# Kernel tuning notes

Hardware: AMD Instinct MI355X
Metric: run time of the kernel (lower is better)

## Reference

```python
import jax, jax.numpy as jnp
import numpy as np

B, S, D, O, R, E = 4, 2048, 4096, 4096, 16, 8
SCALING = 32.0 / 16.0  # lora_alpha / lora_rank


def setup_inputs() -> dict:
    key = jax.random.key(0)
    ks = jax.random.split(key, 7)
    x = jax.random.normal(ks[0], (B, S, D), dtype=jnp.float32)
    W_base = jax.random.normal(ks[1], (O, D), dtype=jnp.float32) * 0.02
    b_base = jnp.zeros((O,), dtype=jnp.float32)
    A_w = jax.random.normal(ks[2], (R, D), dtype=jnp.float32) * 0.02     # lora_A weight
    B_w = jax.random.normal(ks[3], (O, R), dtype=jnp.float32) * 0.02     # lora_B weight
    router_w = jax.random.normal(ks[4], (E, D), dtype=jnp.float32) * 0.02  # router weight (core_router=False -> acts on x)
    cores = jax.random.normal(ks[5], (E, R, R), dtype=jnp.float32)       # expert rank x rank cores
    return {"x": x, "W_base": W_base, "b_base": b_base, "A_w": A_w,
            "B_w": B_w, "router_w": router_w, "cores": cores}


def reference(x, W_base, b_base, A_w, B_w, router_w, cores):
    # base linear: [B,S,O]
    result = jnp.einsum('bsd,od->bso', x, W_base) + b_base
    # lora down-projection (dropout=0 -> identity): [B,S,R]
    ax = jnp.einsum('bsd,rd->bsr', x, A_w)
    # router on x (core_router=False): softmax over experts -> [B,S,E]
    probs = jax.nn.softmax(jnp.einsum('bsd,ed->bse', x, router_w), axis=-1)
    # per-token weighted core applied to ax WITHOUT materializing [B,S,R,R]:
    # first ax through each expert core [B,S,E,R], then weight-reduce over experts.
    per_expert = jnp.einsum('bsr,erq->bseq', ax, cores)
    mixed = jnp.einsum('bseq,bse->bsq', per_expert, probs)  # [B,S,R]
    result = result + jnp.einsum('bsr,or->bso', mixed, B_w) * SCALING
    return result
```

## Files before the change

kernel.cpp:

```cpp
#include <hip/hip_runtime.h>
#include <stdint.h>

#define D_DIM 4096
#define O_DIM 4096
#define M_DIM 8192
#define SCALE_F 2.0f
#define BK 32
#define NKT 128

typedef __attribute__((ext_vector_type(4))) float f32x4;
typedef __attribute__((ext_vector_type(8))) __bf16 bf16x8;
typedef __attribute__((ext_vector_type(8))) unsigned short u16x8;

__device__ __forceinline__ unsigned short f32_to_bf16_bits(float f) {
    union { float f; uint32_t u; } v; v.f = f;
    return (unsigned short)((v.u + 0x7FFFu + ((v.u >> 16) & 1u)) >> 16);
}

__device__ __forceinline__ float dot4(f32x4 a, f32x4 b) {
    return fmaf(a.x, b.x, fmaf(a.y, b.y, fmaf(a.z, b.z, a.w * b.w)));
}

__device__ __forceinline__ int swz(int b) { return b ^ (((b >> 7) & 7) << 4); }

__global__ __launch_bounds__(256) void convert_bf16_kernel(const float* __restrict__ src,
                                                           unsigned short* __restrict__ dst,
                                                           int n4) {
    int stride = gridDim.x * blockDim.x;
    for (int i = blockIdx.x * blockDim.x + threadIdx.x; i < n4; i += stride) {
        f32x4 v = ((const f32x4*)src)[i];
        ushort4 o;
        o.x = f32_to_bf16_bits(v.x);
        o.y = f32_to_bf16_bits(v.y);
        o.z = f32_to_bf16_bits(v.z);
        o.w = f32_to_bf16_bits(v.w);
        ((ushort4*)dst)[i] = o;
    }
}

__global__ __launch_bounds__(256) void partial_mixed_kernel(const float* __restrict__ x,
                                                            const float* __restrict__ A_w,
                                                            const float* __restrict__ router_w,
                                                            unsigned short* __restrict__ xbf,
                                                            float* __restrict__ ypart) {
    __shared__ __align__(16) float Xc[32][132];
    __shared__ __align__(16) float Wc[24][132];

    const int tid = threadIdx.x;
    const int t0 = blockIdx.x * 32;
    const int d0 = blockIdx.y * 512;

    const int tg = tid >> 3;
    const int og = tid & 7;
    float acc0 = 0.f, acc1 = 0.f, acc2 = 0.f;

    for (int sub = 0; sub < 4; ++sub) {
        const int dbase = d0 + sub * 128;
        __syncthreads();
        #pragma unroll
        for (int i = 0; i < 4; ++i) {
            int idx = i * 256 + tid;
            int t = idx >> 5, dq = idx & 31;
            f32x4 v = *(const f32x4*)&x[(size_t)(t0 + t) * D_DIM + dbase + dq * 4];
            *(f32x4*)&Xc[t][dq * 4] = v;
            ushort4 o;
            o.x = f32_to_bf16_bits(v.x);
            o.y = f32_to_bf16_bits(v.y);
            o.z = f32_to_bf16_bits(v.z);
            o.w = f32_to_bf16_bits(v.w);
            *(ushort4*)&xbf[(size_t)(t0 + t) * D_DIM + dbase + dq * 4] = o;
        }
        #pragma unroll
        for (int i = 0; i < 3; ++i) {
            int idx = i * 256 + tid;
            int r = idx >> 5, dq = idx & 31;
            const float* src = (r < 16) ? (A_w + (size_t)r * D_DIM)
                                        : (router_w + (size_t)(r - 16) * D_DIM);
            *(f32x4*)&Wc[r][dq * 4] = *(const f32x4*)&src[dbase + dq * 4];
        }
        __syncthreads();
        #pragma unroll
        for (int dq = 0; dq < 32; ++dq) {
            f32x4 xv = *(const f32x4*)&Xc[tg][dq * 4];
            acc0 += dot4(xv, *(const f32x4*)&Wc[og * 3 + 0][dq * 4]);
            acc1 += dot4(xv, *(const f32x4*)&Wc[og * 3 + 1][dq * 4]);
            acc2 += dot4(xv, *(const f32x4*)&Wc[og * 3 + 2][dq * 4]);
        }
    }
    float* dst = ypart + (((size_t)blockIdx.y * 256 + blockIdx.x) * 32 + tg) * 24 + og * 3;
    dst[0] = acc0; dst[1] = acc1; dst[2] = acc2;
}

__global__ __launch_bounds__(128) void finalize_mixed_kernel(const float* __restrict__ ypart,
                                                             const float* __restrict__ cores,
                                                             float* __restrict__ mixbuf) {
    __shared__ __align__(16) float Cs[2048];
    const int tid = threadIdx.x;
    #pragma unroll
    for (int i = 0; i < 4; ++i) {
        int idx = i * 128 + tid;
        ((f32x4*)Cs)[idx] = ((const f32x4*)cores)[idx];
    }
    __syncthreads();

    const int tok = blockIdx.x * 128 + tid;
    const int tile = tok >> 5, t = tok & 31;

    float y[24];
    #pragma unroll
    for (int j = 0; j < 24; ++j) y[j] = 0.f;
    for (int ds = 0; ds < 8; ++ds) {
        const float* src = ypart + (((size_t)ds * 256 + tile) * 32 + t) * 24;
        #pragma unroll
        for (int j = 0; j < 24; ++j) y[j] += src[j];
    }

    float mx = y[16];
    #pragma unroll
    for (int e = 1; e < 8; ++e) mx = fmaxf(mx, y[16 + e]);
    float p[8], psum = 0.f;
    #pragma unroll
    for (int e = 0; e < 8; ++e) { p[e] = __expf(y[16 + e] - mx); psum += p[e]; }
    const float inv = 1.0f / psum;

    float outq[16];
    #pragma unroll
    for (int q = 0; q < 16; ++q) outq[q] = 0.f;
    for (int e = 0; e < 8; ++e) {
        const float pe = p[e] * inv;
        #pragma unroll
        for (int r = 0; r < 16; ++r) {
            const float ar = y[r] * pe;
            #pragma unroll
            for (int q = 0; q < 16; ++q)
                outq[q] = fmaf(ar, Cs[(e * 16 + r) * 16 + q], outq[q]);
        }
    }
    #pragma unroll
    for (int q = 0; q < 4; ++q) {
        f32x4 v = {outq[q * 4 + 0], outq[q * 4 + 1], outq[q * 4 + 2], outq[q * 4 + 3]};
        *(f32x4*)&mixbuf[(size_t)tok * 16 + q * 4] = v;
    }
}

__global__ __launch_bounds__(512, 2) void gemm_kernel(const unsigned short* __restrict__ xbf,
                                                      const unsigned short* __restrict__ wbf,
                                                      const float* __restrict__ bias,
                                                      const float* __restrict__ Bw,
                                                      const float* __restrict__ mixbuf,
                                                      float* __restrict__ out) {
    __shared__ __align__(16) unsigned short lds[4][2][256 * 32];

    const int bid = blockIdx.x;
    const int xcd = bid & 7;
    const int lid = bid >> 3;
    const int tm = (lid >> 4) * 8 + xcd;
    const int tn = lid & 15;
    const int m0 = tm * 256, n0 = tn * 256;

    const int tid = threadIdx.x;
    const int wave = tid >> 6, lane = tid & 63;
    const int wr = wave >> 2, wcn = wave & 3;

    int aoff[2], boff[2];
    #pragma unroll
    for (int u = 0; u < 2; ++u) {
        int c = u * 512 + tid;
        int g = swz(c * 16);
        int grow = g >> 6, gc8 = (g >> 4) & 3;
        aoff[u] = (m0 + grow) * D_DIM + gc8 * 8;
        boff[u] = (n0 + grow) * D_DIM + gc8 * 8;
    }

    const int tA = lane & 15, kq = lane >> 4;
    int aRd[8], bRd[4];
    #pragma unroll
    for (int mi = 0; mi < 8; ++mi)
        aRd[mi] = swz((wr * 128 + mi * 16 + tA) * 64 + kq * 16);
    #pragma unroll
    for (int ni = 0; ni < 4; ++ni)
        bRd[ni] = swz((wcn * 64 + ni * 16 + tA) * 64 + kq * 16);

    f32x4 acc[8][4];
    const f32x4 fz = {0.f, 0.f, 0.f, 0.f};
    #pragma unroll
    for (int mi = 0; mi < 8; ++mi)
        #pragma unroll
        for (int ni = 0; ni < 4; ++ni) acc[mi][ni] = fz;

#define STAGE_UNIT(sb, kt, u, isA)                                                        \
    do {                                                                                  \
        const unsigned short* gsrc =                                                      \
            (isA) ? (xbf + aoff[u] + (kt)*BK) : (wbf + boff[u] + (kt)*BK);                \
        __builtin_amdgcn_global_load_lds(                                                 \
            (const __attribute__((address_space(1))) void*)gsrc,                          \
            (__attribute__((address_space(3))) void*)(&lds[sb][(isA) ? 0 : 1]             \
                                                         [((u)*512 + wave * 64) * 8]),    \
            16, 0, 0);                                                                    \
    } while (0)

    #pragma unroll
    for (int kt = 0; kt < 3; ++kt) {
        STAGE_UNIT(kt, kt, 0, 1);
        STAGE_UNIT(kt, kt, 1, 1);
        STAGE_UNIT(kt, kt, 0, 0);
        STAGE_UNIT(kt, kt, 1, 0);
    }
    asm volatile("s_waitcnt vmcnt(8)" ::: "memory");
    __builtin_amdgcn_s_barrier();
    asm volatile("" ::: "memory");

    for (int jj = 0; jj < 32; ++jj) {
        #pragma unroll
        for (int i = 0; i < 4; ++i) {
            const int j = jj * 4 + i;
            const int buf = i;
            const int kt = j + 3;
            const int sbuf = (i + 3) & 3;
            const char* Ab = (const char*)&lds[buf][0][0];
            const char* Bb = (const char*)&lds[buf][1][0];

            bf16x8 b0 = __builtin_bit_cast(bf16x8, *(const u16x8*)(Bb + bRd[0]));
            bf16x8 b1 = __builtin_bit_cast(bf16x8, *(const u16x8*)(Bb + bRd[1]));
            bf16x8 b2 = __builtin_bit_cast(bf16x8, *(const u16x8*)(Bb + bRd[2]));
            bf16x8 b3 = __builtin_bit_cast(bf16x8, *(const u16x8*)(Bb + bRd[3]));
            bf16x8 a0 = __builtin_bit_cast(bf16x8, *(const u16x8*)(Ab + aRd[0]));
            bf16x8 a1 = __builtin_bit_cast(bf16x8, *(const u16x8*)(Ab + aRd[1]));
            bf16x8 a2 = __builtin_bit_cast(bf16x8, *(const u16x8*)(Ab + aRd[2]));
            bf16x8 a3 = __builtin_bit_cast(bf16x8, *(const u16x8*)(Ab + aRd[3]));
            if (kt < NKT) {
                STAGE_UNIT(sbuf, kt, 0, 1);
                STAGE_UNIT(sbuf, kt, 1, 1);
                STAGE_UNIT(sbuf, kt, 0, 0);
                STAGE_UNIT(sbuf, kt, 1, 0);
            }
            asm volatile("" ::: "memory");
            __builtin_amdgcn_s_barrier();
            asm volatile("s_waitcnt lgkmcnt(0)" ::: "memory");
            __builtin_amdgcn_s_setprio(1);
            acc[0][0] = __builtin_amdgcn_mfma_f32_16x16x32_bf16(a0, b0, acc[0][0], 0, 0, 0);
            acc[0][1] = __builtin_amdgcn_mfma_f32_16x16x32_bf16(a0, b1, acc[0][1], 0, 0, 0);
            acc[0][2] = __builtin_amdgcn_mfma_f32_16x16x32_bf16(a0, b2, acc[0][2], 0, 0, 0);
            acc[0][3] = __builtin_amdgcn_mfma_f32_16x16x32_bf16(a0, b3, acc[0][3], 0, 0, 0);
            acc[1][0] = __builtin_amdgcn_mfma_f32_16x16x32_bf16(a1, b0, acc[1][0], 0, 0, 0);
            acc[1][1] = __builtin_amdgcn_mfma_f32_16x16x32_bf16(a1, b1, acc[1][1], 0, 0, 0);
            acc[1][2] = __builtin_amdgcn_mfma_f32_16x16x32_bf16(a1, b2, acc[1][2], 0, 0, 0);
            acc[1][3] = __builtin_amdgcn_mfma_f32_16x16x32_bf16(a1, b3, acc[1][3], 0, 0, 0);
            acc[2][0] = __builtin_amdgcn_mfma_f32_16x16x32_bf16(a2, b0, acc[2][0], 0, 0, 0);
            acc[2][1] = __builtin_amdgcn_mfma_f32_16x16x32_bf16(a2, b1, acc[2][1], 0, 0, 0);
            acc[2][2] = __builtin_amdgcn_mfma_f32_16x16x32_bf16(a2, b2, acc[2][2], 0, 0, 0);
            acc[2][3] = __builtin_amdgcn_mfma_f32_16x16x32_bf16(a2, b3, acc[2][3], 0, 0, 0);
            acc[3][0] = __builtin_amdgcn_mfma_f32_16x16x32_bf16(a3, b0, acc[3][0], 0, 0, 0);
            acc[3][1] = __builtin_amdgcn_mfma_f32_16x16x32_bf16(a3, b1, acc[3][1], 0, 0, 0);
            acc[3][2] = __builtin_amdgcn_mfma_f32_16x16x32_bf16(a3, b2, acc[3][2], 0, 0, 0);
            acc[3][3] = __builtin_amdgcn_mfma_f32_16x16x32_bf16(a3, b3, acc[3][3], 0, 0, 0);
            __builtin_amdgcn_s_setprio(0);

            bf16x8 a4 = __builtin_bit_cast(bf16x8, *(const u16x8*)(Ab + aRd[4]));
            bf16x8 a5 = __builtin_bit_cast(bf16x8, *(const u16x8*)(Ab + aRd[5]));
            bf16x8 a6 = __builtin_bit_cast(bf16x8, *(const u16x8*)(Ab + aRd[6]));
            bf16x8 a7 = __builtin_bit_cast(bf16x8, *(const u16x8*)(Ab + aRd[7]));
            asm volatile("s_waitcnt lgkmcnt(0)" ::: "memory");
            __builtin_amdgcn_s_setprio(1);
            acc[4][0] = __builtin_amdgcn_mfma_f32_16x16x32_bf16(a4, b0, acc[4][0], 0, 0, 0);
            acc[4][1] = __builtin_amdgcn_mfma_f32_16x16x32_bf16(a4, b1, acc[4][1], 0, 0, 0);
            acc[4][2] = __builtin_amdgcn_mfma_f32_16x16x32_bf16(a4, b2, acc[4][2], 0, 0, 0);
            acc[4][3] = __builtin_amdgcn_mfma_f32_16x16x32_bf16(a4, b3, acc[4][3], 0, 0, 0);
            acc[5][0] = __builtin_amdgcn_mfma_f32_16x16x32_bf16(a5, b0, acc[5][0], 0, 0, 0);
            acc[5][1] = __builtin_amdgcn_mfma_f32_16x16x32_bf16(a5, b1, acc[5][1], 0, 0, 0);
            acc[5][2] = __builtin_amdgcn_mfma_f32_16x16x32_bf16(a5, b2, acc[5][2], 0, 0, 0);
            acc[5][3] = __builtin_amdgcn_mfma_f32_16x16x32_bf16(a5, b3, acc[5][3], 0, 0, 0);
            acc[6][0] = __builtin_amdgcn_mfma_f32_16x16x32_bf16(a6, b0, acc[6][0], 0, 0, 0);
            acc[6][1] = __builtin_amdgcn_mfma_f32_16x16x32_bf16(a6, b1, acc[6][1], 0, 0, 0);
            acc[6][2] = __builtin_amdgcn_mfma_f32_16x16x32_bf16(a6, b2, acc[6][2], 0, 0, 0);
            acc[6][3] = __builtin_amdgcn_mfma_f32_16x16x32_bf16(a6, b3, acc[6][3], 0, 0, 0);
            acc[7][0] = __builtin_amdgcn_mfma_f32_16x16x32_bf16(a7, b0, acc[7][0], 0, 0, 0);
            acc[7][1] = __builtin_amdgcn_mfma_f32_16x16x32_bf16(a7, b1, acc[7][1], 0, 0, 0);
            acc[7][2] = __builtin_amdgcn_mfma_f32_16x16x32_bf16(a7, b2, acc[7][2], 0, 0, 0);
            acc[7][3] = __builtin_amdgcn_mfma_f32_16x16x32_bf16(a7, b3, acc[7][3], 0, 0, 0);
            __builtin_amdgcn_s_setprio(0);
            asm volatile("s_waitcnt vmcnt(8)" ::: "memory");
            __builtin_amdgcn_s_barrier();
            asm volatile("" ::: "memory");
        }
    }
#undef STAGE_UNIT

    const int colq = lane & 15, rq = lane >> 4;
    f32x4 bwv[4][4];
    float bcol[4];
    #pragma unroll
    for (int ni = 0; ni < 4; ++ni) {
        const int col = n0 + wcn * 64 + ni * 16 + colq;
        bcol[ni] = bias[col];
        #pragma unroll
        for (int k = 0; k < 4; ++k) bwv[ni][k] = *(const f32x4*)&Bw[(size_t)col * 16 + k * 4];
    }
    #pragma unroll
    for (int mi = 0; mi < 8; ++mi) {
        #pragma unroll
        for (int j = 0; j < 4; ++j) {
            const int row = m0 + wr * 128 + mi * 16 + rq * 4 + j;
            const f32x4* mx = (const f32x4*)&mixbuf[(size_t)row * 16];
            const f32x4 m0v = mx[0], m1v = mx[1], m2v = mx[2], m3v = mx[3];
            #pragma unroll
            for (int ni = 0; ni < 4; ++ni) {
                const int col = n0 + wcn * 64 + ni * 16 + colq;
                const float lora = dot4(m0v, bwv[ni][0]) + dot4(m1v, bwv[ni][1]) +
                                   dot4(m2v, bwv[ni][2]) + dot4(m3v, bwv[ni][3]);
                out[(size_t)row * O_DIM + col] = acc[mi][ni][j] + bcol[ni] + SCALE_F * lora;
            }
        }
    }
}

extern "C" void kernel_launch(void* const* d_in, const int* in_sizes, int n_in,
                              void* d_out, int out_size, void* d_ws, size_t ws_size,
                              hipStream_t stream) {
    const float* x        = (const float*)d_in[0];
    const float* W_base   = (const float*)d_in[1];
    const float* b_base   = (const float*)d_in[2];
    const float* A_w      = (const float*)d_in[3];
    const float* B_w      = (const float*)d_in[4];
    const float* router_w = (const float*)d_in[5];
    const float* cores    = (const float*)d_in[6];
    float* out = (float*)d_out;

    char* ws = (char*)d_ws;
    unsigned short* xbf = (unsigned short*)ws;
    unsigned short* wbf = (unsigned short*)(ws + (size_t)M_DIM * D_DIM * 2);
    char* after_w = ws + (size_t)M_DIM * D_DIM * 2 + (size_t)O_DIM * D_DIM * 2;
    float* mixbuf = (float*)after_w;
    float* ypart  = (float*)(after_w + (size_t)M_DIM * 16 * 4);

    convert_bf16_kernel<<<2048, 256, 0, stream>>>(W_base, wbf, (O_DIM * D_DIM) / 4);
    partial_mixed_kernel<<<dim3(256, 8), 256, 0, stream>>>(x, A_w, router_w, xbf, ypart);
    finalize_mixed_kernel<<<64, 128, 0, stream>>>(ypart, cores, mixbuf);
    gemm_kernel<<<512, 512, 0, stream>>>(xbf, wbf, b_base, B_w, mixbuf, out);
}
```

Measured before the change: 345.5 us.

## Merge W conversion with partial mixing kernel and split GEMM k-loop staging

Folds the W_base bf16 conversion and the x down-projection/router partials into one launch, with blocks split by index, so the two independent prologue jobs run concurrently and one launch is saved. The GEMM main loop is reorganised: B and A tile prefetches are issued in two halves around an extra barrier. The final four k-steps are peeled out with shrinking vmcnt waits instead of a per-iteration kt<NKT branch. The extra barrier per k-step may cost more than the finer interleaving gains.

```diff
diff --git a/kernel.cpp b/kernel.cpp
--- a/kernel.cpp
+++ b/kernel.cpp
@@ -23,32 +23,36 @@
 
 __device__ __forceinline__ int swz(int b) { return b ^ (((b >> 7) & 7) << 4); }
 
-__global__ __launch_bounds__(256) void convert_bf16_kernel(const float* __restrict__ src,
-                                                           unsigned short* __restrict__ dst,
-                                                           int n4) {
-    int stride = gridDim.x * blockDim.x;
-    for (int i = blockIdx.x * blockDim.x + threadIdx.x; i < n4; i += stride) {
-        f32x4 v = ((const f32x4*)src)[i];
-        ushort4 o;
-        o.x = f32_to_bf16_bits(v.x);
-        o.y = f32_to_bf16_bits(v.y);
-        o.z = f32_to_bf16_bits(v.z);
-        o.w = f32_to_bf16_bits(v.w);
-        ((ushort4*)dst)[i] = o;
-    }
-}
-
-__global__ __launch_bounds__(256) void partial_mixed_kernel(const float* __restrict__ x,
-                                                            const float* __restrict__ A_w,
-                                                            const float* __restrict__ router_w,
-                                                            unsigned short* __restrict__ xbf,
-                                                            float* __restrict__ ypart) {
+__global__ __launch_bounds__(256) void pre_kernel(const float* __restrict__ x,
+                                                  const float* __restrict__ W_base,
+                                                  const float* __restrict__ A_w,
+                                                  const float* __restrict__ router_w,
+                                                  unsigned short* __restrict__ xbf,
+                                                  unsigned short* __restrict__ wbf,
+                                                  float* __restrict__ ypart) {
     __shared__ __align__(16) float Xc[32][132];
     __shared__ __align__(16) float Wc[24][132];
 
     const int tid = threadIdx.x;
-    const int t0 = blockIdx.x * 32;
-    const int d0 = blockIdx.y * 512;
+
+    if (blockIdx.x < 2048) {
+        const int n4 = (O_DIM * D_DIM) / 4;
+        const int stride = 2048 * 256;
+        for (int i = blockIdx.x * 256 + tid; i < n4; i += stride) {
+            f32x4 v = ((const f32x4*)W_base)[i];
+            ushort4 o;
+            o.x = f32_to_bf16_bits(v.x);
+            o.y = f32_to_bf16_bits(v.y);
+            o.z = f32_to_bf16_bits(v.z);
+            o.w = f32_to_bf16_bits(v.w);
+            ((ushort4*)wbf)[i] = o;
+        }
+        return;
+    }
+
+    const int b = blockIdx.x - 2048;
+    const int t0 = (b & 255) * 32;
+    const int d0 = (b >> 8) * 512;
 
     const int tg = tid >> 3;
     const int og = tid & 7;
@@ -87,7 +91,7 @@
             acc2 += dot4(xv, *(const f32x4*)&Wc[og * 3 + 2][dq * 4]);
         }
     }
-    float* dst = ypart + (((size_t)blockIdx.y * 256 + blockIdx.x) * 32 + tg) * 24 + og * 3;
+    float* dst = ypart + (((size_t)(b >> 8) * 256 + (b & 255)) * 32 + tg) * 24 + og * 3;
     dst[0] = acc0; dst[1] = acc1; dst[2] = acc2;
 }
 
@@ -199,6 +203,80 @@
             16, 0, 0);                                                                    \
     } while (0)
 
+#define K_ITER(BUF, SBUF, KT, STG, VMC)                                                   \
+    {                                                                                     \
+        const char* Ab = (const char*)&lds[BUF][0][0];                                    \
+        const char* Bb = (const char*)&lds[BUF][1][0];                                    \
+        bf16x8 b0 = __builtin_bit_cast(bf16x8, *(const u16x8*)(Bb + bRd[0]));             \
+        bf16x8 b1 = __builtin_bit_cast(bf16x8, *(const u16x8*)(Bb + bRd[1]));             \
+        bf16x8 b2 = __builtin_bit_cast(bf16x8, *(const u16x8*)(Bb + bRd[2]));             \
+        bf16x8 b3 = __builtin_bit_cast(bf16x8, *(const u16x8*)(Bb + bRd[3]));             \
+        bf16x8 a0 = __builtin_bit_cast(bf16x8, *(const u16x8*)(Ab + aRd[0]));             \
+        bf16x8 a1 = __builtin_bit_cast(bf16x8, *(const u16x8*)(Ab + aRd[1]));             \
+        bf16x8 a2 = __builtin_bit_cast(bf16x8, *(const u16x8*)(Ab + aRd[2]));             \
+        bf16x8 a3 = __builtin_bit_cast(bf16x8, *(const u16x8*)(Ab + aRd[3]));             \
+        if (STG) {                                                                        \
+            STAGE_UNIT(SBUF, KT, 0, 1);                                                   \
+            STAGE_UNIT(SBUF, KT, 1, 1);                                                   \
+        }                                                                                 \
+        asm volatile("" ::: "memory");                                                    \
+        __builtin_amdgcn_s_barrier();                                                     \
+        asm volatile("s_waitcnt lgkmcnt(0)" ::: "memory");                                \
+        __builtin_amdgcn_s_setprio(1);                                                    \
+        acc[0][0] = __builtin_amdgcn_mfma_f32_16x16x32_bf16(a0, b0, acc[0][0], 0, 0, 0);  \
+        acc[0][1] = __builtin_amdgcn_mfma_f32_16x16x32_bf16(a0, b1, acc[0][1], 0, 0, 0);  \
+        acc[0][2] = __builtin_amdgcn_mfma_f32_16x16x32_bf16(a0, b2, acc[0][2], 0, 0, 0);  \
+        acc[0][3] = __builtin_amdgcn_mfma_f32_16x16x32_bf16(a0, b3, acc[0][3], 0, 0, 0);  \
+        acc[1][0] = __builtin_amdgcn_mfma_f32_16x16x32_bf16(a1, b0, acc[1][0], 0, 0, 0);  \
+        acc[1][1] = __builtin_amdgcn_mfma_f32_16x16x32_bf16(a1, b1, acc[1][1], 0, 0, 0);  \
+        acc[1][2] = __builtin_amdgcn_mfma_f32_16x16x32_bf16(a1, b2, acc[1][2], 0, 0, 0);  \
+        acc[1][3] = __builtin_amdgcn_mfma_f32_16x16x32_bf16(a1, b3, acc[1][3], 0, 0, 0);  \
+        acc[2][0] = __builtin_amdgcn_mfma_f32_16x16x32_bf16(a2, b0, acc[2][0], 0, 0, 0);  \
+        acc[2][1] = __builtin_amdgcn_mfma_f32_16x16x32_bf16(a2, b1, acc[2][1], 0, 0, 0);  \
+        acc[2][2] = __builtin_amdgcn_mfma_f32_16x16x32_bf16(a2, b2, acc[2][2], 0, 0, 0);  \
+        acc[2][3] = __builtin_amdgcn_mfma_f32_16x16x32_bf16(a2, b3, acc[2][3], 0, 0, 0);  \
+        acc[3][0] = __builtin_amdgcn_mfma_f32_16x16x32_bf16(a3, b0, acc[3][0], 0, 0, 0);  \
+        acc[3][1] = __builtin_amdgcn_mfma_f32_16x16x32_bf16(a3, b1, acc[3][1], 0, 0, 0);  \
+        acc[3][2] = __builtin_amdgcn_mfma_f32_16x16x32_bf16(a3, b2, acc[3][2], 0, 0, 0);  \
+        acc[3][3] = __builtin_amdgcn_mfma_f32_16x16x32_bf16(a3, b3, acc[3][3], 0, 0, 0);  \
+        __builtin_amdgcn_s_setprio(0);                                                    \
+        asm volatile("" ::: "memory");                                                    \
+        __builtin_amdgcn_s_barrier();                                                     \
+        asm volatile("" ::: "memory");                                                    \
+        bf16x8 a4 = __builtin_bit_cast(bf16x8, *(const u16x8*)(Ab + aRd[4]));             \
+        bf16x8 a5 = __builtin_bit_cast(bf16x8, *(const u16x8*)(Ab + aRd[5]));             \
+        bf16x8 a6 = __builtin_bit_cast(bf16x8, *(const u16x8*)(Ab + aRd[6]));             \
+        bf16x8 a7 = __builtin_bit_cast(bf16x8, *(const u16x8*)(Ab + aRd[7]));             \
+        if (STG) {                                                                        \
+            STAGE_UNIT(SBUF, KT, 0, 0);                                                   \
+            STAGE_UNIT(SBUF, KT, 1, 0);                                                   \
+        }                                                                                 \
+        asm volatile("s_waitcnt vmcnt(" #VMC ")" ::: "memory");                           \
+        __builtin_amdgcn_s_barrier();                                                     \
+        asm volatile("s_waitcnt lgkmcnt(0)" ::: "memory");                                \
+        __builtin_amdgcn_s_setprio(1);                                                    \
+        acc[4][0] = __builtin_amdgcn_mfma_f32_16x16x32_bf16(a4, b0, acc[4][0], 0, 0, 0);  \
+        acc[4][1] = __builtin_amdgcn_mfma_f32_16x16x32_bf16(a4, b1, acc[4][1], 0, 0, 0);  \
+        acc[4][2] = __builtin_amdgcn_mfma_f32_16x16x32_bf16(a4, b2, acc[4][2], 0, 0, 0);  \
+        acc[4][3] = __builtin_amdgcn_mfma_f32_16x16x32_bf16(a4, b3, acc[4][3], 0, 0, 0);  \
+        acc[5][0] = __builtin_amdgcn_mfma_f32_16x16x32_bf16(a5, b0, acc[5][0], 0, 0, 0);  \
+        acc[5][1] = __builtin_amdgcn_mfma_f32_16x16x32_bf16(a5, b1, acc[5][1], 0, 0, 0);  \
+        acc[5][2] = __builtin_amdgcn_mfma_f32_16x16x32_bf16(a5, b2, acc[5][2], 0, 0, 0);  \
+        acc[5][3] = __builtin_amdgcn_mfma_f32_16x16x32_bf16(a5, b3, acc[5][3], 0, 0, 0);  \
+        acc[6][0] = __builtin_amdgcn_mfma_f32_16x16x32_bf16(a6, b0, acc[6][0], 0, 0, 0);  \
+        acc[6][1] = __builtin_amdgcn_mfma_f32_16x16x32_bf16(a6, b1, acc[6][1], 0, 0, 0);  \
+        acc[6][2] = __builtin_amdgcn_mfma_f32_16x16x32_bf16(a6, b2, acc[6][2], 0, 0, 0);  \
+        acc[6][3] = __builtin_amdgcn_mfma_f32_16x16x32_bf16(a6, b3, acc[6][3], 0, 0, 0);  \
+        acc[7][0] = __builtin_amdgcn_mfma_f32_16x16x32_bf16(a7, b0, acc[7][0], 0, 0, 0);  \
+        acc[7][1] = __builtin_amdgcn_mfma_f32_16x16x32_bf16(a7, b1, acc[7][1], 0, 0, 0);  \
+        acc[7][2] = __builtin_amdgcn_mfma_f32_16x16x32_bf16(a7, b2, acc[7][2], 0, 0, 0);  \
+        acc[7][3] = __builtin_amdgcn_mfma_f32_16x16x32_bf16(a7, b3, acc[7][3], 0, 0, 0);  \
+        __builtin_amdgcn_s_setprio(0);                                                    \
+        asm volatile("" ::: "memory");                                                    \
+        __builtin_amdgcn_s_barrier();                                                     \
+        asm volatile("" ::: "memory");                                                    \
+    }
+
     #pragma unroll
     for (int kt = 0; kt < 3; ++kt) {
         STAGE_UNIT(kt, kt, 0, 1);
@@ -210,80 +288,19 @@
     __builtin_amdgcn_s_barrier();
     asm volatile("" ::: "memory");
 
-    for (int jj = 0; jj < 32; ++jj) {
+    for (int jj = 0; jj < 31; ++jj) {
         #pragma unroll
         for (int i = 0; i < 4; ++i) {
             const int j = jj * 4 + i;
-            const int buf = i;
             const int kt = j + 3;
-            const int sbuf = (i + 3) & 3;
-            const char* Ab = (const char*)&lds[buf][0][0];
-            const char* Bb = (const char*)&lds[buf][1][0];
-
-            bf16x8 b0 = __builtin_bit_cast(bf16x8, *(const u16x8*)(Bb + bRd[0]));
-            bf16x8 b1 = __builtin_bit_cast(bf16x8, *(const u16x8*)(Bb + bRd[1]));
-            bf16x8 b2 = __builtin_bit_cast(bf16x8, *(const u16x8*)(Bb + bRd[2]));
-            bf16x8 b3 = __builtin_bit_cast(bf16x8, *(const u16x8*)(Bb + bRd[3]));
-            bf16x8 a0 = __builtin_bit_cast(bf16x8, *(const u16x8*)(Ab + aRd[0]));
-            bf16x8 a1 = __builtin_bit_cast(bf16x8, *(const u16x8*)(Ab + aRd[1]));
-            bf16x8 a2 = __builtin_bit_cast(bf16x8, *(const u16x8*)(Ab + aRd[2]));
-            bf16x8 a3 = __builtin_bit_cast(bf16x8, *(const u16x8*)(Ab + aRd[3]));
-            if (kt < NKT) {
-                STAGE_UNIT(sbuf, kt, 0, 1);
-                STAGE_UNIT(sbuf, kt, 1, 1);
-                STAGE_UNIT(sbuf, kt, 0, 0);
-                STAGE_UNIT(sbuf, kt, 1, 0);
-            }
-            asm volatile("" ::: "memory");
-            __builtin_amdgcn_s_barrier();
-            asm volatile("s_waitcnt lgkmcnt(0)" ::: "memory");
-            __builtin_amdgcn_s_setprio(1);
-            acc[0][0] = __builtin_amdgcn_mfma_f32_16x16x32_bf16(a0, b0, acc[0][0], 0, 0, 0);
-            acc[0][1] = __builtin_amdgcn_mfma_f32_16x16x32_bf16(a0, b1, acc[0][1], 0, 0, 0);
-            acc[0][2] = __builtin_amdgcn_mfma_f32_16x16x32_bf16(a0, b2, acc[0][2], 0, 0, 0);
-            acc[0][3] = __builtin_amdgcn_mfma_f32_16x16x32_bf16(a0, b3, acc[0][3], 0, 0, 0);
-            acc[1][0] = __builtin_amdgcn_mfma_f32_16x16x32_bf16(a1, b0, acc[1][0], 0, 0, 0);
-            acc[1][1] = __builtin_amdgcn_mfma_f32_16x16x32_bf16(a1, b1, acc[1][1], 0, 0, 0);
-            acc[1][2] = __builtin_amdgcn_mfma_f32_16x16x32_bf16(a1, b2, acc[1][2], 0, 0, 0);
-            acc[1][3] = __builtin_amdgcn_mfma_f32_16x16x32_bf16(a1, b3, acc[1][3], 0, 0, 0);
-            acc[2][0] = __builtin_amdgcn_mfma_f32_16x16x32_bf16(a2, b0, acc[2][0], 0, 0, 0);
-            acc[2][1] = __builtin_amdgcn_mfma_f32_16x16x32_bf16(a2, b1, acc[2][1], 0, 0, 0);
-            acc[2][2] = __builtin_amdgcn_mfma_f32_16x16x32_bf16(a2, b2, acc[2][2], 0, 0, 0);
-            acc[2][3] = __builtin_amdgcn_mfma_f32_16x16x32_bf16(a2, b3, acc[2][3], 0, 0, 0);
-            acc[3][0] = __builtin_amdgcn_mfma_f32_16x16x32_bf16(a3, b0, acc[3][0], 0, 0, 0);
-            acc[3][1] = __builtin_amdgcn_mfma_f32_16x16x32_bf16(a3, b1, acc[3][1], 0, 0, 0);
-            acc[3][2] = __builtin_amdgcn_mfma_f32_16x16x32_bf16(a3, b2, acc[3][2], 0, 0, 0);
-            acc[3][3] = __builtin_amdgcn_mfma_f32_16x16x32_bf16(a3, b3, acc[3][3], 0, 0, 0);
-            __builtin_amdgcn_s_setprio(0);
-
-            bf16x8 a4 = __builtin_bit_cast(bf16x8, *(const u16x8*)(Ab + aRd[4]));
-            bf16x8 a5 = __builtin_bit_cast(bf16x8, *(const u16x8*)(Ab + aRd[5]));
-            bf16x8 a6 = __builtin_bit_cast(bf16x8, *(const u16x8*)(Ab + aRd[6]));
-            bf16x8 a7 = __builtin_bit_cast(bf16x8, *(const u16x8*)(Ab + aRd[7]));
-            asm volatile("s_waitcnt lgkmcnt(0)" ::: "memory");
-            __builtin_amdgcn_s_setprio(1);
-            acc[4][0] = __builtin_amdgcn_mfma_f32_16x16x32_bf16(a4, b0, acc[4][0], 0, 0, 0);
-            acc[4][1] = __builtin_amdgcn_mfma_f32_16x16x32_bf16(a4, b1, acc[4][1], 0, 0, 0);
-            acc[4][2] = __builtin_amdgcn_mfma_f32_16x16x32_bf16(a4, b2, acc[4][2], 0, 0, 0);
-            acc[4][3] = __builtin_amdgcn_mfma_f32_16x16x32_bf16(a4, b3, acc[4][3], 0, 0, 0);
-            acc[5][0] = __builtin_amdgcn_mfma_f32_16x16x32_bf16(a5, b0, acc[5][0], 0, 0, 0);
-            acc[5][1] = __builtin_amdgcn_mfma_f32_16x16x32_bf16(a5, b1, acc[5][1], 0, 0, 0);
-            acc[5][2] = __builtin_amdgcn_mfma_f32_16x16x32_bf16(a5, b2, acc[5][2], 0, 0, 0);
-            acc[5][3] = __builtin_amdgcn_mfma_f32_16x16x32_bf16(a5, b3, acc[5][3], 0, 0, 0);
-            acc[6][0] = __builtin_amdgcn_mfma_f32_16x16x32_bf16(a6, b0, acc[6][0], 0, 0, 0);
-            acc[6][1] = __builtin_amdgcn_mfma_f32_16x16x32_bf16(a6, b1, acc[6][1], 0, 0, 0);
-            acc[6][2] = __builtin_amdgcn_mfma_f32_16x16x32_bf16(a6, b2, acc[6][2], 0, 0, 0);
-            acc[6][3] = __builtin_amdgcn_mfma_f32_16x16x32_bf16(a6, b3, acc[6][3], 0, 0, 0);
-            acc[7][0] = __builtin_amdgcn_mfma_f32_16x16x32_bf16(a7, b0, acc[7][0], 0, 0, 0);
-            acc[7][1] = __builtin_amdgcn_mfma_f32_16x16x32_bf16(a7, b1, acc[7][1], 0, 0, 0);
-            acc[7][2] = __builtin_amdgcn_mfma_f32_16x16x32_bf16(a7, b2, acc[7][2], 0, 0, 0);
-            acc[7][3] = __builtin_amdgcn_mfma_f32_16x16x32_bf16(a7, b3, acc[7][3], 0, 0, 0);
-            __builtin_amdgcn_s_setprio(0);
-            asm volatile("s_waitcnt vmcnt(8)" ::: "memory");
-            __builtin_amdgcn_s_barrier();
-            asm volatile("" ::: "memory");
-        }
-    }
+            K_ITER(i, (i + 3) & 3, kt, 1, 8);
+        }
+    }
+    K_ITER(0, 3, 127, 1, 8);
+    K_ITER(1, 0, 0, 0, 4);
+    K_ITER(2, 0, 0, 0, 0);
+    K_ITER(3, 0, 0, 0, 0);
+#undef K_ITER
 #undef STAGE_UNIT
 
     const int colq = lane & 15, rq = lane >> 4;
@@ -333,8 +350,7 @@
     float* mixbuf = (float*)after_w;
     float* ypart  = (float*)(after_w + (size_t)M_DIM * 16 * 4);
 
-    convert_bf16_kernel<<<2048, 256, 0, stream>>>(W_base, wbf, (O_DIM * D_DIM) / 4);
-    partial_mixed_kernel<<<dim3(256, 8), 256, 0, stream>>>(x, A_w, router_w, xbf, ypart);
+    pre_kernel<<<4096, 256, 0, stream>>>(x, W_base, A_w, router_w, xbf, wbf, ypart);
     finalize_mixed_kernel<<<64, 128, 0, stream>>>(ypart, cores, mixbuf);
     gemm_kernel<<<512, 512, 0, stream>>>(xbf, wbf, b_base, B_w, mixbuf, out);
 }
```

After: 357.2 us. +3.4%, slower.
